# Performance work log

Hardware: AMD Instinct MI355X
Metric: run time of the kernel (lower is better)

## Reference

```python
import jax, jax.numpy as jnp
import numpy as np

# Conv2d_mvm config (matches init_kwargs): the bit-sliced crossbar MVM is a
# fixed-point emulation of an exact stride-1 conv2d with padding=1, no bias.
C_IN, C_OUT, K, H, W, PAD = 16, 16, 3, 1024, 1024, 1


def setup_inputs() -> dict:
    key = jax.random.key(0)
    kx, kw = jax.random.split(key)
    x = jax.random.normal(kx, (1, C_IN, H, W), dtype=jnp.float32)
    # kaiming_uniform-style init for the conv weight
    fan_in = C_IN * K * K
    bound = 1.0 / np.sqrt(fan_in)
    weight = jax.random.uniform(kw, (C_OUT, C_IN, K, K), dtype=jnp.float32,
                                minval=-bound, maxval=bound)
    return {"x": x, "weight": weight}


def reference(x, weight):
    # Ideal math of the bit-sliced crossbar MVM: per output pixel, the
    # flattened (C_in*K*K) receptive field dotted with each flattened filter.
    out = jax.lax.conv_general_dilated(
        x, weight,
        window_strides=(1, 1),
        padding=((PAD, PAD), (PAD, PAD)),
        dimension_numbers=("NCHW", "OIHW", "NCHW"),
    )
    # Original forward returns (C_out, H_out, W_out) with batch=1 assumed.
    return out[0]
```

## Files before the change

kernel.cpp:

```cpp
#include <hip/hip_runtime.h>


#define H 1024
#define W 1024
#define HW (H * W)
#define TW 128
#define TH 8
#define LROWS 10
#define NQ 34
#define NJOBS (LROWS * NQ)
#define LCOLS 130
#define LPITCH (LCOLS * 32)
#define LDS_BYTES (LROWS * LPITCH)

typedef __bf16 bf16x8 __attribute__((ext_vector_type(8)));
typedef float f32x4 __attribute__((ext_vector_type(4)));
typedef unsigned short ushort8 __attribute__((ext_vector_type(8)));
typedef unsigned int uint4v __attribute__((ext_vector_type(4)));

__device__ __host__ inline unsigned short f2bf(float f) {
  unsigned u = __builtin_bit_cast(unsigned, f);
  return (unsigned short)((u + 0x7fffu + ((u >> 16) & 1u)) >> 16);
}

__device__ __forceinline__ void stage_job(int j, const float* __restrict__ x,
                                          int colbase, int rowbase, char* lds) {
  const int ly  = j / NQ;
  const int qx  = j - ly * NQ;
  const int gy  = rowbase - 1 + ly;
  const float rowm = ((unsigned)gy < (unsigned)H) ? 1.f : 0.f;
  const int gyc  = gy < 0 ? 0 : (gy > H - 1 ? H - 1 : gy);
  const int gx0  = colbase - 4 + 4 * qx;
  const int gx0c = gx0 < 0 ? 0 : (gx0 > W - 4 ? W - 4 : gx0);
  const unsigned voff = (unsigned)((gyc * W + gx0c) * 4);

  f32x4 L[16];
  asm volatile(
      "global_load_dwordx4 %0, %8, %9\n\t"
      "global_load_dwordx4 %1, %8, %10\n\t"
      "global_load_dwordx4 %2, %8, %11\n\t"
      "global_load_dwordx4 %3, %8, %12\n\t"
      "global_load_dwordx4 %4, %8, %13\n\t"
      "global_load_dwordx4 %5, %8, %14\n\t"
      "global_load_dwordx4 %6, %8, %15\n\t"
      "global_load_dwordx4 %7, %8, %16\n\t"
      : "=&v"(L[0]), "=&v"(L[1]), "=&v"(L[2]), "=&v"(L[3]),
        "=&v"(L[4]), "=&v"(L[5]), "=&v"(L[6]), "=&v"(L[7])
      : "v"(voff), "s"(x), "s"(x + HW), "s"(x + 2 * HW), "s"(x + 3 * HW),
        "s"(x + 4 * HW), "s"(x + 5 * HW), "s"(x + 6 * HW), "s"(x + 7 * HW));
  asm volatile(
      "global_load_dwordx4 %0, %8, %9\n\t"
      "global_load_dwordx4 %1, %8, %10\n\t"
      "global_load_dwordx4 %2, %8, %11\n\t"
      "global_load_dwordx4 %3, %8, %12\n\t"
      "global_load_dwordx4 %4, %8, %13\n\t"
      "global_load_dwordx4 %5, %8, %14\n\t"
      "global_load_dwordx4 %6, %8, %15\n\t"
      "global_load_dwordx4 %7, %8, %16\n\t"
      : "=&v"(L[8]), "=&v"(L[9]), "=&v"(L[10]), "=&v"(L[11]),
        "=&v"(L[12]), "=&v"(L[13]), "=&v"(L[14]), "=&v"(L[15])
      : "v"(voff), "s"(x + 8 * HW), "s"(x + 9 * HW), "s"(x + 10 * HW),
        "s"(x + 11 * HW), "s"(x + 12 * HW), "s"(x + 13 * HW),
        "s"(x + 14 * HW), "s"(x + 15 * HW));

  asm volatile("s_waitcnt vmcnt(0)" ::: "memory");
  __builtin_amdgcn_sched_barrier(0);

#pragma unroll
  for (int i = 0; i < 4; ++i) {
    const int gx = gx0 + i;
    const int lx = gx - (colbase - 1);
    if ((unsigned)lx < (unsigned)LCOLS) {
      const float fm = rowm * (((unsigned)gx < (unsigned)W) ? 1.f : 0.f);
      const int lb = (ly * LPITCH + lx * 32) ^ (((lx >> 2) & 3) << 4);
#pragma unroll
      for (int h = 0; h < 2; ++h) {
        uint4v d;
#pragma unroll
        for (int p = 0; p < 4; ++p) {
          const unsigned lo = f2bf(L[h * 8 + 2 * p][i] * fm);
          const unsigned hi = f2bf(L[h * 8 + 2 * p + 1][i] * fm);
          d[p] = lo | (hi << 16);
        }
        *(uint4v*)(lds + (lb ^ (h << 4))) = d;
      }
    }
  }
}

__global__ __launch_bounds__(256) void conv_mfma(
    const float* __restrict__ x, const float* __restrict__ w,
    float* __restrict__ out) {
  __shared__ __align__(16) char lds[LDS_BYTES];

  const int tid  = threadIdx.x;
  const int lane = tid & 63;
  const int wave = tid >> 6;
  const int m = lane & 15;
  const int q = lane >> 4;
  const int colbase = blockIdx.x * TW;
  const int rowbase = blockIdx.y * TH;

  stage_job(tid, x, colbase, rowbase, lds);
  if (tid < NJOBS - 256) stage_job(256 + tid, x, colbase, rowbase, lds);

  ushort8 wU[5];
  {
    const int tq = q >> 1, ci0 = (q & 1) * 8;
#pragma unroll
    for (int p = 0; p < 5; ++p) {
      const int t = 2 * p + tq;
      ushort8 u;
#pragma unroll
      for (int j = 0; j < 8; ++j) {
        float v = (t <= 8) ? w[m * 144 + (ci0 + j) * 9 + t] : 0.f;
        u[j] = f2bf(v);
      }
      wU[p] = u;
    }
  }

  int baseaddr[5];
#pragma unroll
  for (int p = 0; p < 5; ++p) {
    int t = 2 * p + (q >> 1);
    int ky = 0, kx = 0;
    if (t <= 8) { ky = t / 3; kx = t - ky * 3; }
    int col = m + kx;
    int b = ky * LPITCH + col * 32 + (q & 1) * 16;
    b ^= ((col >> 2) & 3) << 4;
    baseaddr[p] = b + wave * 2 * LPITCH;
  }

  __syncthreads();

#pragma unroll
  for (int r = 0; r < 2; ++r) {
#pragma unroll
    for (int g = 0; g < 8; ++g) {
      f32x4 acc = {0.f, 0.f, 0.f, 0.f};
#pragma unroll
      for (int p = 0; p < 5; ++p) {
        ushort8 bU = *(const ushort8*)(lds + (baseaddr[p] + r * LPITCH + g * 512));
        acc = __builtin_amdgcn_mfma_f32_16x16x32_bf16(
            __builtin_bit_cast(bf16x8, bU),
            __builtin_bit_cast(bf16x8, wU[p]),
            acc, 0, 0, 0);
      }
      const int y  = rowbase + wave * 2 + r;
      const int x0 = colbase + g * 16 + q * 4;
      *(f32x4*)(out + m * HW + y * W + x0) = acc;
    }
  }
}

extern "C" void kernel_launch(void* const* d_in, const int* in_sizes, int n_in,
                              void* d_out, int out_size, void* d_ws, size_t ws_size,
                              hipStream_t stream) {
  const float* x = (const float*)d_in[0];
  const float* w = (const float*)d_in[1];
  float* out = (float*)d_out;

  dim3 grid(W / TW, H / TH);
  conv_mfma<<<grid, 256, 0, stream>>>(x, w, out);
}
```

Before: 42.11 us.

## Halve tile height, prepack bf16 weights in a prep kernel, raise occupancy

Reduces the output tile from 8 to 4 rows per block, so each wave computes one row and LDS per block shrinks. This doubles the block count and raises the halo overhead from 10/8 to 6/4 rows. A separate prep kernel converts the weights to bf16 in MFMA fragment layout once per call, so each block loads five vectors instead of doing strided gathers and conversions. Launch bounds request 6 waves per SIMD. The cost is an extra kernel launch and more redundant halo loads.

```diff
diff --git a/kernel.cpp b/kernel.cpp
--- a/kernel.cpp
+++ b/kernel.cpp
@@ -5,8 +5,8 @@
 #define W 1024
 #define HW (H * W)
 #define TW 128
-#define TH 8
-#define LROWS 10
+#define TH 4
+#define LROWS 6
 #define NQ 34
 #define NJOBS (LROWS * NQ)
 #define LCOLS 130
@@ -21,6 +21,21 @@
 __device__ __host__ inline unsigned short f2bf(float f) {
   unsigned u = __builtin_bit_cast(unsigned, f);
   return (unsigned short)((u + 0x7fffu + ((u >> 16) & 1u)) >> 16);
+}
+
+__global__ __launch_bounds__(256) void conv_prep(const float* __restrict__ w,
+                                                 unsigned short* __restrict__ wA) {
+  int i = blockIdx.x * 256 + threadIdx.x;
+  if (i >= 5 * 64 * 8) return;
+  int j = i & 7;
+  int l = (i >> 3) & 63;
+  int p = i >> 9;
+  int k = (l >> 4) * 8 + j;
+  int t = 2 * p + (k >> 4);
+  int ci = k & 15;
+  int co = l & 15;
+  float v = (t <= 8) ? w[co * 144 + ci * 9 + t] : 0.f;
+  wA[i] = f2bf(v);
 }
 
 __device__ __forceinline__ void stage_job(int j, const float* __restrict__ x,
@@ -88,8 +103,8 @@
   }
 }
 
-__global__ __launch_bounds__(256) void conv_mfma(
-    const float* __restrict__ x, const float* __restrict__ w,
+__global__ __launch_bounds__(256, 6) void conv_mfma(
+    const float* __restrict__ x, const unsigned short* __restrict__ wA,
     float* __restrict__ out) {
   __shared__ __align__(16) char lds[LDS_BYTES];
 
@@ -101,24 +116,12 @@
   const int colbase = blockIdx.x * TW;
   const int rowbase = blockIdx.y * TH;
 
-  stage_job(tid, x, colbase, rowbase, lds);
-  if (tid < NJOBS - 256) stage_job(256 + tid, x, colbase, rowbase, lds);
+  if (tid < NJOBS) stage_job(tid, x, colbase, rowbase, lds);
 
   ushort8 wU[5];
-  {
-    const int tq = q >> 1, ci0 = (q & 1) * 8;
 #pragma unroll
-    for (int p = 0; p < 5; ++p) {
-      const int t = 2 * p + tq;
-      ushort8 u;
-#pragma unroll
-      for (int j = 0; j < 8; ++j) {
-        float v = (t <= 8) ? w[m * 144 + (ci0 + j) * 9 + t] : 0.f;
-        u[j] = f2bf(v);
-      }
-      wU[p] = u;
-    }
-  }
+  for (int p = 0; p < 5; ++p)
+    wU[p] = *(const ushort8*)&wA[(p * 64 + lane) * 8];
 
   int baseaddr[5];
 #pragma unroll
@@ -129,28 +132,25 @@
     int col = m + kx;
     int b = ky * LPITCH + col * 32 + (q & 1) * 16;
     b ^= ((col >> 2) & 3) << 4;
-    baseaddr[p] = b + wave * 2 * LPITCH;
+    baseaddr[p] = b + wave * LPITCH;
   }
 
   __syncthreads();
 
 #pragma unroll
-  for (int r = 0; r < 2; ++r) {
+  for (int g = 0; g < 8; ++g) {
+    f32x4 acc = {0.f, 0.f, 0.f, 0.f};
 #pragma unroll
-    for (int g = 0; g < 8; ++g) {
-      f32x4 acc = {0.f, 0.f, 0.f, 0.f};
-#pragma unroll
-      for (int p = 0; p < 5; ++p) {
-        ushort8 bU = *(const ushort8*)(lds + (baseaddr[p] + r * LPITCH + g * 512));
-        acc = __builtin_amdgcn_mfma_f32_16x16x32_bf16(
-            __builtin_bit_cast(bf16x8, bU),
-            __builtin_bit_cast(bf16x8, wU[p]),
-            acc, 0, 0, 0);
-      }
-      const int y  = rowbase + wave * 2 + r;
-      const int x0 = colbase + g * 16 + q * 4;
-      *(f32x4*)(out + m * HW + y * W + x0) = acc;
+    for (int p = 0; p < 5; ++p) {
+      ushort8 bU = *(const ushort8*)(lds + (baseaddr[p] + g * 512));
+      acc = __builtin_amdgcn_mfma_f32_16x16x32_bf16(
+          __builtin_bit_cast(bf16x8, bU),
+          __builtin_bit_cast(bf16x8, wU[p]),
+          acc, 0, 0, 0);
     }
+    const int y  = rowbase + wave;
+    const int x0 = colbase + g * 16 + q * 4;
+    *(f32x4*)(out + m * HW + y * W + x0) = acc;
   }
 }
 
@@ -160,7 +160,10 @@
   const float* x = (const float*)d_in[0];
   const float* w = (const float*)d_in[1];
   float* out = (float*)d_out;
+  unsigned short* wA = (unsigned short*)d_ws;
+
+  conv_prep<<<10, 256, 0, stream>>>(w, wA);
 
   dim3 grid(W / TW, H / TH);
-  conv_mfma<<<grid, 256, 0, stream>>>(x, w, out);
+  conv_mfma<<<grid, 256, 0, stream>>>(x, wA, out);
 }
```

Measured after the change: 37.29 us (median of 2 runs). 11.4% less time.
